# Optimization experiments

Hardware: AMD Instinct MI355X
Metric: run time of the kernel (lower is better)

Reference implementation:

```python
import jax, jax.numpy as jnp
import numpy as np

EPS = 1e-08


def _l2norm(x):
    return x / (jnp.linalg.norm(x, axis=-1, keepdims=True) + EPS)


def _mlp(x, weights):
    # weights: list of (W, b); gelu between layers, none after last
    n = len(weights)
    for i, (W, b) in enumerate(weights):
        x = x @ W + b
        if i < n - 1:
            x = jax.nn.gelu(x)  # approximate gelu, matches jax.nn.gelu default
    return x


def setup_inputs() -> dict:
    key = jax.random.key(0)
    ks = jax.random.split(key, 16)
    N, A, L, K = 65536, 32, 256, 1024
    enc_dims = [A, 512, 1024, L]
    dec_dims = [L, 1024, 512, A]

    def lin(k, din, dout):
        kw, kb = jax.random.split(k)
        W = jax.random.normal(kw, (din, dout), jnp.float32) / np.sqrt(din)
        b = jnp.zeros((dout,), jnp.float32)
        return W, b

    inp = {}
    inp["action"] = jax.random.normal(ks[0], (N, A), jnp.float32)
    inp["dim_weights"] = jax.random.uniform(ks[1], (A,), jnp.float32)
    for i in range(3):
        W, b = lin(ks[2 + i], enc_dims[i], enc_dims[i + 1])
        inp[f"enc_w{i}"], inp[f"enc_b{i}"] = W, b
    for i in range(3):
        W, b = lin(ks[5 + i], dec_dims[i], dec_dims[i + 1])
        inp[f"dec_w{i}"], inp[f"dec_b{i}"] = W, b
    cb = jax.random.normal(ks[8], (K, L), jnp.float32) * 0.1
    inp["codebook"] = _l2norm(cb)
    return inp


def reference(action, dim_weights,
              enc_w0, enc_b0, enc_w1, enc_b1, enc_w2, enc_b2,
              dec_w0, dec_b0, dec_w1, dec_b1, dec_w2, dec_b2,
              codebook):
    enc = [(enc_w0, enc_b0), (enc_w1, enc_b1), (enc_w2, enc_b2)]
    dec = [(dec_w0, dec_b0), (dec_w1, dec_b1), (dec_w2, dec_b2)]

    z_e = _l2norm(_mlp(action, enc))                       # [N, L]
    cb = _l2norm(codebook)                                 # [K, L]
    # squared euclidean distances [N, K]
    dists = (jnp.sum(z_e * z_e, axis=-1, keepdims=True)
             - 2.0 * z_e @ cb.T
             + jnp.sum(cb * cb, axis=-1))
    code_idx = jnp.argmin(dists, axis=-1)                  # [N]
    z_q = cb[code_idx]                                     # [N, L]

    z_q_ste = z_e + jax.lax.stop_gradient(z_q - z_e)
    action_hat = _mlp(z_q_ste, dec)                        # [N, A]

    sq_err = (action - action_hat) ** 2 * dim_weights
    recon_loss = jnp.mean(sq_err)
    codebook_loss = jnp.mean((jax.lax.stop_gradient(z_e) - z_q) ** 2)
    commit_loss = jnp.mean((z_e - jax.lax.stop_gradient(z_q)) ** 2)
    return action_hat, code_idx, recon_loss, codebook_loss, commit_loss
```

## Files before the change

kernel.cpp:

```cpp
#include <hip/hip_runtime.h>
#include <math.h>

#define N_ROWS 65536

typedef short short8 __attribute__((ext_vector_type(8)));
typedef float f32x4 __attribute__((ext_vector_type(4)));

__device__ __forceinline__ float gelu_f(float x) {
  float x3 = x * x * x;
  float t = tanhf(0.7978845608028654f * (x + 0.044715f * x3));
  return 0.5f * x * (1.0f + t);
}

__device__ __forceinline__ unsigned short f2bf(float f) {
  unsigned u = __float_as_uint(f);
  unsigned r = u + 0x7fffu + ((u >> 16) & 1u);
  return (unsigned short)(r >> 16);
}
__device__ __forceinline__ float bf2f(unsigned short h) {
  return __uint_as_float(((unsigned)h) << 16);
}

__device__ __forceinline__ void split3(float v, unsigned short& p0,
                                       unsigned short& p1, unsigned short& p2) {
  p0 = f2bf(v);
  float r = v - bf2f(p0);
  p1 = f2bf(r);
  r -= bf2f(p1);
  p2 = f2bf(r);
}

__device__ __forceinline__ void split3f(float v, unsigned short& p0,
                                        unsigned short& p1, unsigned short& p2) {
  unsigned u = __float_as_uint(v);
  unsigned h0 = (u + 0x8000u) & 0xffff0000u;
  float r = v - __uint_as_float(h0);
  unsigned u1 = __float_as_uint(r);
  unsigned h1 = (u1 + 0x8000u) & 0xffff0000u;
  float r2 = r - __uint_as_float(h1);
  p0 = (unsigned short)(h0 >> 16);
  p1 = (unsigned short)(h1 >> 16);
  p2 = f2bf(r2);
}

__device__ __forceinline__ void split2f(float v, unsigned short& p0,
                                        unsigned short& p1) {
  unsigned u = __float_as_uint(v);
  unsigned h0 = (u + 0x8000u) & 0xffff0000u;
  float r = v - __uint_as_float(h0);
  p0 = (unsigned short)(h0 >> 16);
  p1 = f2bf(r);
}

__device__ __forceinline__ f32x4 mfma16(short8 a, short8 b, f32x4 c) {
  return __builtin_amdgcn_mfma_f32_16x16x32_bf16(a, b, c, 0, 0, 0);
}

template <bool GELU>
__global__ __launch_bounds__(256) void gemm_kernel(
    const float* __restrict__ A, const float* __restrict__ W,
    const float* __restrict__ bias, float* __restrict__ C,
    int din, int dout) {
  __shared__ float As[16][132];
  __shared__ float Ws[16][132];
  int t = threadIdx.x;
  int tx = t & 15, ty = t >> 4;
  int c0 = blockIdx.x * 128;
  int r0 = blockIdx.y * 128;

  float acc[8][8];
#pragma unroll
  for (int i = 0; i < 8; ++i)
#pragma unroll
    for (int j = 0; j < 8; ++j) acc[i][j] = 0.0f;

  int kchunks = din >> 4;
  for (int kc = 0; kc < kchunks; ++kc) {
    int k0 = kc << 4;
    __syncthreads();
#pragma unroll
    for (int it = 0; it < 2; ++it) {
      int id = t + it * 256;
      int r = id >> 2;
      int kq = (id & 3) * 4;
      float4 v = *(const float4*)&A[(long)(r0 + r) * din + (k0 + kq)];
      As[kq + 0][r] = v.x; As[kq + 1][r] = v.y;
      As[kq + 2][r] = v.z; As[kq + 3][r] = v.w;
      int k = id >> 5;
      int cq = (id & 31) * 4;
      float4 w = *(const float4*)&W[(long)(k0 + k) * dout + (c0 + cq)];
      *(float4*)&Ws[k][cq] = w;
    }
    __syncthreads();
#pragma unroll
    for (int k = 0; k < 16; ++k) {
      float av[8], bv[8];
      *(float4*)&av[0] = *(const float4*)&As[k][ty * 4];
      *(float4*)&av[4] = *(const float4*)&As[k][ty * 4 + 64];
      *(float4*)&bv[0] = *(const float4*)&Ws[k][tx * 4];
      *(float4*)&bv[4] = *(const float4*)&Ws[k][tx * 4 + 64];
#pragma unroll
      for (int i = 0; i < 8; ++i)
#pragma unroll
        for (int j = 0; j < 8; ++j)
          acc[i][j] = fmaf(av[i], bv[j], acc[i][j]);
    }
  }

  float bbv[8];
  *(float4*)&bbv[0] = *(const float4*)&bias[c0 + tx * 4];
  *(float4*)&bbv[4] = *(const float4*)&bias[c0 + tx * 4 + 64];
#pragma unroll
  for (int i = 0; i < 8; ++i) {
    long row = r0 + ty * 4 + (i & 3) + ((i >> 2) * 64);
    float o[8];
#pragma unroll
    for (int j = 0; j < 8; ++j) {
      float v = acc[i][j] + bbv[j];
      o[j] = GELU ? gelu_f(v) : v;
    }
    *(float4*)&C[row * dout + c0 + tx * 4] = *(float4*)&o[0];
    *(float4*)&C[row * dout + c0 + tx * 4 + 64] = *(float4*)&o[4];
  }
}

template <bool GELU>
__global__ __launch_bounds__(256) void gemm64_kernel(
    const float* __restrict__ A, const float* __restrict__ W,
    const float* __restrict__ bias, float* __restrict__ C,
    int din, int dout) {
  __shared__ float As[16][68];
  __shared__ float Ws[16][68];
  int t = threadIdx.x;
  int tx = t & 15, ty = t >> 4;
  int c0 = blockIdx.x * 64;
  int r0 = blockIdx.y * 64;

  float acc[4][4];
#pragma unroll
  for (int i = 0; i < 4; ++i)
#pragma unroll
    for (int j = 0; j < 4; ++j) acc[i][j] = 0.0f;

  int kchunks = din >> 4;
  for (int kc = 0; kc < kchunks; ++kc) {
    int k0 = kc << 4;
    __syncthreads();
    {
      int r = t >> 2, kq = (t & 3) * 4;
      float4 v = *(const float4*)&A[(long)(r0 + r) * din + (k0 + kq)];
      As[kq + 0][r] = v.x; As[kq + 1][r] = v.y;
      As[kq + 2][r] = v.z; As[kq + 3][r] = v.w;
      int k = t >> 4, cq = (t & 15) * 4;
      *(float4*)&Ws[k][cq] = *(const float4*)&W[(long)(k0 + k) * dout + (c0 + cq)];
    }
    __syncthreads();
#pragma unroll
    for (int k = 0; k < 16; ++k) {
      float av[4], bv[4];
      *(float4*)&av[0] = *(const float4*)&As[k][ty * 4];
      *(float4*)&bv[0] = *(const float4*)&Ws[k][tx * 4];
#pragma unroll
      for (int i = 0; i < 4; ++i)
#pragma unroll
        for (int j = 0; j < 4; ++j)
          acc[i][j] = fmaf(av[i], bv[j], acc[i][j]);
    }
  }

  float4 bb = *(const float4*)&bias[c0 + tx * 4];
#pragma unroll
  for (int i = 0; i < 4; ++i) {
    long row = r0 + ty * 4 + i;
    float o[4];
    o[0] = acc[i][0] + bb.x; o[1] = acc[i][1] + bb.y;
    o[2] = acc[i][2] + bb.z; o[3] = acc[i][3] + bb.w;
    if (GELU) {
      o[0] = gelu_f(o[0]); o[1] = gelu_f(o[1]);
      o[2] = gelu_f(o[2]); o[3] = gelu_f(o[3]);
    }
    *(float4*)&C[row * dout + c0 + tx * 4] = *(float4*)&o[0];
  }
}

__global__ void frag_pack_kernel(const float* __restrict__ W,
                                 unsigned short* __restrict__ Bf,
                                 int K, int N) {
  int l = threadIdx.x;
  int m = l & 15, q = l >> 4;
  int cb = blockIdx.x, kb = blockIdx.y;
  unsigned short s0[8], s1[8], s2[8];
#pragma unroll
  for (int j = 0; j < 8; ++j) {
    float v = W[(long)(kb * 32 + q * 8 + j) * N + cb * 16 + m];
    split3(v, s0[j], s1[j], s2[j]);
  }
  size_t base = ((size_t)cb * (K / 32) + kb) * 3 * 512;
  *(short8*)&Bf[base + 0 * 512 + l * 8] = *(short8*)s0;
  *(short8*)&Bf[base + 1 * 512 + l * 8] = *(short8*)s1;
  *(short8*)&Bf[base + 2 * 512 + l * 8] = *(short8*)s2;
}

__global__ void frag_pack2_t(const float* __restrict__ cbn,
                             unsigned short* __restrict__ Bf) {
  int l = threadIdx.x;
  int m = l & 15, q = l >> 4;
  int cb = blockIdx.x, kb = blockIdx.y;
  unsigned short s0[8], s1[8];
  const float* src = cbn + (long)(cb * 16 + m) * 256 + kb * 32 + q * 8;
#pragma unroll
  for (int j = 0; j < 8; ++j) split2f(src[j], s0[j], s1[j]);
  size_t base = ((size_t)(cb * 8 + kb) * 2) * 512;
  *(short8*)&Bf[base + l * 8] = *(short8*)s0;
  *(short8*)&Bf[base + 512 + l * 8] = *(short8*)s1;
}

template <bool GELU>
__global__ __launch_bounds__(256) void mfma3_gemm(
    const float* __restrict__ A, const unsigned short* __restrict__ Bf,
    const float* __restrict__ bias, float* __restrict__ C,
    int K, int dout) {
  __shared__ unsigned short A_f[3 * 2 * 4 * 512];
  int t = threadIdx.x;
  int lane = t & 63, wave = t >> 6;
  int q = lane >> 4, m = lane & 15;
  int wrb = wave >> 1;
  int wr = wrb * 64, wc = (wave & 1) * 64;

  int gx = gridDim.x, tot = gx * gridDim.y;
  int lin = blockIdx.y * gx + blockIdx.x;
  if (!(tot & 7)) lin = (lin & 7) * (tot >> 3) + (lin >> 3);
  int bx = lin % gx, by = lin / gx;

  long r0 = (long)by * 128;
  int c0 = bx * 128;
  int kchunks = K >> 5;

  f32x4 acc[4][4];
#pragma unroll
  for (int i = 0; i < 4; ++i)
#pragma unroll
    for (int j = 0; j < 4; ++j) acc[i][j] = (f32x4){0.f, 0.f, 0.f, 0.f};

  int rs = t >> 1, hs = (t & 1) * 16;
  const float* aptr = A + (r0 + rs) * K + hs;
  int cb0 = (c0 + wc) >> 4;
  int xw = (rs >> 4) & 3, wrbw = rs >> 6, mw = rs & 15;
  int g0 = ((t & 1) * 2 + 0) * 16 + mw;
  int g1 = ((t & 1) * 2 + 1) * 16 + mw;
  int wb0 = (0 * 2 + wrbw) * 4 + xw;
  int wb1 = (1 * 2 + wrbw) * 4 + xw;
  int wb2 = (2 * 2 + wrbw) * 4 + xw;

  for (int kb = 0; kb < kchunks; ++kb) {
    __syncthreads();
    {
      int kt = kb << 5;
      float fv[16];
      *(float4*)&fv[0] = *(const float4*)(aptr + kt + 0);
      *(float4*)&fv[4] = *(const float4*)(aptr + kt + 4);
      *(float4*)&fv[8] = *(const float4*)(aptr + kt + 8);
      *(float4*)&fv[12] = *(const float4*)(aptr + kt + 12);
      unsigned short a0[16], a1[16], a2[16];
#pragma unroll
      for (int i = 0; i < 16; ++i) split3f(fv[i], a0[i], a1[i], a2[i]);
      *(uint4*)&A_f[wb0 * 512 + g0 * 8] = ((uint4*)a0)[0];
      *(uint4*)&A_f[wb0 * 512 + g1 * 8] = ((uint4*)a0)[1];
      *(uint4*)&A_f[wb1 * 512 + g0 * 8] = ((uint4*)a1)[0];
      *(uint4*)&A_f[wb1 * 512 + g1 * 8] = ((uint4*)a1)[1];
      *(uint4*)&A_f[wb2 * 512 + g0 * 8] = ((uint4*)a2)[0];
      *(uint4*)&A_f[wb2 * 512 + g1 * 8] = ((uint4*)a2)[1];
    }
    __syncthreads();
    short8 af[3][4];
#pragma unroll
    for (int p = 0; p < 3; ++p)
#pragma unroll
      for (int x = 0; x < 4; ++x)
        af[p][x] = *(const short8*)&A_f[((p * 2 + wrb) * 4 + x) * 512 + lane * 8];
#pragma unroll
    for (int ct = 0; ct < 4; ++ct) {
      size_t fb = ((size_t)(cb0 + ct) * kchunks + kb) * 3 * 512 + lane * 8;
      short8 b0 = *(const short8*)&Bf[fb];
      short8 b1 = *(const short8*)&Bf[fb + 512];
      short8 b2 = *(const short8*)&Bf[fb + 1024];
#pragma unroll
      for (int rt = 0; rt < 4; ++rt) {
        acc[rt][ct] = mfma16(af[0][rt], b0, acc[rt][ct]);
        acc[rt][ct] = mfma16(af[0][rt], b1, acc[rt][ct]);
        acc[rt][ct] = mfma16(af[1][rt], b0, acc[rt][ct]);
        acc[rt][ct] = mfma16(af[0][rt], b2, acc[rt][ct]);
        acc[rt][ct] = mfma16(af[1][rt], b1, acc[rt][ct]);
        acc[rt][ct] = mfma16(af[2][rt], b0, acc[rt][ct]);
      }
    }
  }

#pragma unroll
  for (int ct = 0; ct < 4; ++ct) {
    long col = c0 + wc + ct * 16 + m;
    float bv = bias[col];
#pragma unroll
    for (int rt = 0; rt < 4; ++rt) {
      long rowb = r0 + wr + rt * 16 + q * 4;
#pragma unroll
      for (int r = 0; r < 4; ++r) {
        float v = acc[rt][ct][r] + bv;
        if (GELU) v = gelu_f(v);
        C[(rowb + r) * dout + col] = v;
      }
    }
  }
}

__global__ __launch_bounds__(512) void mfma3_norm(
    const float* __restrict__ A, const unsigned short* __restrict__ Bf,
    const float* __restrict__ bias, float* __restrict__ z_e,
    float* __restrict__ ze2) {
  __shared__ unsigned short A_f[3 * 2 * 4 * 512];
  __shared__ float S[128][4];
  __shared__ float Sinv[128];
  const int K = 1024, kchunks = 32;
  int t = threadIdx.x;
  int lane = t & 63, wave = t >> 6;
  int q = lane >> 4, m = lane & 15;
  int wrb = wave >> 2;
  int wcq = wave & 3;
  long r0 = (long)blockIdx.x * 128;

  f32x4 acc[4][4];
#pragma unroll
  for (int i = 0; i < 4; ++i)
#pragma unroll
    for (int j = 0; j < 4; ++j) acc[i][j] = (f32x4){0.f, 0.f, 0.f, 0.f};

  int rs = t >> 2, kq = t & 3;
  const float* aptr = A + (r0 + rs) * K + kq * 8;
  int xw = (rs >> 4) & 3, wrbw = rs >> 6, mw = rs & 15;
  int gw = kq * 16 + mw;
  int wb0 = (0 * 2 + wrbw) * 4 + xw;
  int wb1 = (1 * 2 + wrbw) * 4 + xw;
  int wb2 = (2 * 2 + wrbw) * 4 + xw;
  int cb0 = wcq * 4;

  for (int kb = 0; kb < kchunks; ++kb) {
    __syncthreads();
    {
      float fv[8];
      *(float4*)&fv[0] = *(const float4*)(aptr + (kb << 5));
      *(float4*)&fv[4] = *(const float4*)(aptr + (kb << 5) + 4);
      unsigned short a0[8], a1[8], a2[8];
#pragma unroll
      for (int i = 0; i < 8; ++i) split3f(fv[i], a0[i], a1[i], a2[i]);
      *(uint4*)&A_f[wb0 * 512 + gw * 8] = *(uint4*)a0;
      *(uint4*)&A_f[wb1 * 512 + gw * 8] = *(uint4*)a1;
      *(uint4*)&A_f[wb2 * 512 + gw * 8] = *(uint4*)a2;
    }
    __syncthreads();
    short8 af[3][4];
#pragma unroll
    for (int p = 0; p < 3; ++p)
#pragma unroll
      for (int x = 0; x < 4; ++x)
        af[p][x] = *(const short8*)&A_f[((p * 2 + wrb) * 4 + x) * 512 + lane * 8];
#pragma unroll
    for (int ct = 0; ct < 4; ++ct) {
      size_t fb = ((size_t)(cb0 + ct) * kchunks + kb) * 3 * 512 + lane * 8;
      short8 b0 = *(const short8*)&Bf[fb];
      short8 b1 = *(const short8*)&Bf[fb + 512];
      short8 b2 = *(const short8*)&Bf[fb + 1024];
#pragma unroll
      for (int rt = 0; rt < 4; ++rt) {
        acc[rt][ct] = mfma16(af[0][rt], b0, acc[rt][ct]);
        acc[rt][ct] = mfma16(af[0][rt], b1, acc[rt][ct]);
        acc[rt][ct] = mfma16(af[1][rt], b0, acc[rt][ct]);
        acc[rt][ct] = mfma16(af[0][rt], b2, acc[rt][ct]);
        acc[rt][ct] = mfma16(af[1][rt], b1, acc[rt][ct]);
        acc[rt][ct] = mfma16(af[2][rt], b0, acc[rt][ct]);
      }
    }
  }

#pragma unroll
  for (int ct = 0; ct < 4; ++ct) {
    float bv = bias[wcq * 64 + ct * 16 + m];
#pragma unroll
    for (int rt = 0; rt < 4; ++rt)
#pragma unroll
      for (int r = 0; r < 4; ++r) acc[rt][ct][r] += bv;
  }

#pragma unroll
  for (int rt = 0; rt < 4; ++rt)
#pragma unroll
    for (int r = 0; r < 4; ++r) {
      float s = acc[rt][0][r] * acc[rt][0][r] + acc[rt][1][r] * acc[rt][1][r] +
                acc[rt][2][r] * acc[rt][2][r] + acc[rt][3][r] * acc[rt][3][r];
#pragma unroll
      for (int off = 1; off <= 8; off <<= 1) s += __shfl_xor(s, off);
      if (m == 0) S[wrb * 64 + rt * 16 + q * 4 + r][wcq] = s;
    }
  __syncthreads();
  if (t < 128) {
    float s = S[t][0] + S[t][1] + S[t][2] + S[t][3];
    float den = sqrtf(s) + 1e-8f;
    Sinv[t] = 1.0f / den;
    ze2[r0 + t] = s / (den * den);
  }
  __syncthreads();
#pragma unroll
  for (int rt = 0; rt < 4; ++rt)
#pragma unroll
    for (int r = 0; r < 4; ++r) {
      int rl = wrb * 64 + rt * 16 + q * 4 + r;
      float inv = Sinv[rl];
#pragma unroll
      for (int ct = 0; ct < 4; ++ct)
        z_e[(r0 + rl) * 256 + wcq * 64 + ct * 16 + m] = acc[rt][ct][r] * inv;
    }
}

__global__ __launch_bounds__(256) void dist2_mfma(
    const float* __restrict__ z_e, const unsigned short* __restrict__ cbf,
    int* __restrict__ idxc, int* __restrict__ fixcnt, int* __restrict__ fixlist) {
  __shared__ unsigned short A_f[2 * 8 * 4 * 512];
  __shared__ float Lv1[64][4], Lv2[64][4];
  __shared__ int Lc1[64][4];
  int t = threadIdx.x;
  int lane = t & 63, wave = t >> 6;
  int q = lane >> 4, m = lane & 15;
  long r0 = (long)blockIdx.x * 64;

#pragma unroll
  for (int it = 0; it < 4; ++it) {
    int kb = it * 2 + (t >> 7);
    int rs = (t & 127) >> 1, hs = (t & 1) * 16;
    const float* ap = z_e + (r0 + rs) * 256 + kb * 32 + hs;
    float fv[16];
    *(float4*)&fv[0] = *(const float4*)(ap + 0);
    *(float4*)&fv[4] = *(const float4*)(ap + 4);
    *(float4*)&fv[8] = *(const float4*)(ap + 8);
    *(float4*)&fv[12] = *(const float4*)(ap + 12);
    unsigned short a0[16], a1[16];
#pragma unroll
    for (int i = 0; i < 16; ++i) split2f(fv[i], a0[i], a1[i]);
    int x = rs >> 4, mm = rs & 15;
    int ga = ((t & 1) * 2 + 0) * 16 + mm;
    int gb = ((t & 1) * 2 + 1) * 16 + mm;
    int b0 = ((0 * 8 + kb) * 4 + x) * 512;
    int b1 = ((1 * 8 + kb) * 4 + x) * 512;
    *(uint4*)&A_f[b0 + ga * 8] = ((uint4*)a0)[0];
    *(uint4*)&A_f[b0 + gb * 8] = ((uint4*)a0)[1];
    *(uint4*)&A_f[b1 + ga * 8] = ((uint4*)a1)[0];
    *(uint4*)&A_f[b1 + gb * 8] = ((uint4*)a1)[1];
  }
  __syncthreads();

  float v1[4][4], v2[4][4];
  int c1[4][4];
#pragma unroll
  for (int i = 0; i < 4; ++i)
#pragma unroll
    for (int j = 0; j < 4; ++j) { v1[i][j] = -3.4e38f; v2[i][j] = -3.4e38f; c1[i][j] = 0; }

  for (int ctp = 0; ctp < 4; ++ctp) {
    f32x4 acc[4][4];
#pragma unroll
    for (int i = 0; i < 4; ++i)
#pragma unroll
      for (int j = 0; j < 4; ++j) acc[i][j] = (f32x4){0.f, 0.f, 0.f, 0.f};

    for (int kb = 0; kb < 8; ++kb) {
      short8 af0[4], af1[4];
#pragma unroll
      for (int rt = 0; rt < 4; ++rt) {
        af0[rt] = *(const short8*)&A_f[((0 * 8 + kb) * 4 + rt) * 512 + lane * 8];
        af1[rt] = *(const short8*)&A_f[((1 * 8 + kb) * 4 + rt) * 512 + lane * 8];
      }
      short8 bf0[4], bf1[4];
#pragma unroll
      for (int cs = 0; cs < 4; ++cs) {
        int cb = ctp * 16 + (cs >> 1) * 8 + wave * 2 + (cs & 1);
        size_t fb = ((size_t)(cb * 8 + kb) * 2) * 512 + lane * 8;
        bf0[cs] = *(const short8*)&cbf[fb];
        bf1[cs] = *(const short8*)&cbf[fb + 512];
      }
#pragma unroll
      for (int rt = 0; rt < 4; ++rt)
#pragma unroll
        for (int cs = 0; cs < 4; ++cs) {
          acc[rt][cs] = mfma16(af0[rt], bf0[cs], acc[rt][cs]);
          acc[rt][cs] = mfma16(af0[rt], bf1[cs], acc[rt][cs]);
          acc[rt][cs] = mfma16(af1[rt], bf0[cs], acc[rt][cs]);
        }
    }
#pragma unroll
    for (int rt = 0; rt < 4; ++rt)
#pragma unroll
      for (int cs = 0; cs < 4; ++cs) {
        int colb = ctp * 256 + (cs >> 1) * 128 + wave * 32 + (cs & 1) * 16 + m;
#pragma unroll
        for (int r = 0; r < 4; ++r) {
          float v = acc[rt][cs][r];
          float nv2 = fmaxf(v2[rt][r], fminf(v, v1[rt][r]));
          if (v > v1[rt][r]) { c1[rt][r] = colb; v1[rt][r] = v; }
          v2[rt][r] = nv2;
        }
      }
  }

#pragma unroll
  for (int off = 1; off <= 8; off <<= 1) {
#pragma unroll
    for (int rt = 0; rt < 4; ++rt)
#pragma unroll
      for (int r = 0; r < 4; ++r) {
        float ov1 = __shfl_xor(v1[rt][r], off);
        float ov2 = __shfl_xor(v2[rt][r], off);
        int oc1 = __shfl_xor(c1[rt][r], off);
        float nv2 = fmaxf(fmaxf(v2[rt][r], ov2), fminf(v1[rt][r], ov1));
        if (ov1 > v1[rt][r] || (ov1 == v1[rt][r] && oc1 < c1[rt][r])) {
          v1[rt][r] = ov1; c1[rt][r] = oc1;
        }
        v2[rt][r] = nv2;
      }
  }
  if (m == 0) {
#pragma unroll
    for (int rt = 0; rt < 4; ++rt)
#pragma unroll
      for (int r = 0; r < 4; ++r) {
        int rloc = rt * 16 + q * 4 + r;
        Lv1[rloc][wave] = v1[rt][r];
        Lv2[rloc][wave] = v2[rt][r];
        Lc1[rloc][wave] = c1[rt][r];
      }
  }
  __syncthreads();
  if (t < 64) {
    float a1 = Lv1[t][0], a2 = Lv2[t][0];
    int ac = Lc1[t][0];
#pragma unroll
    for (int w = 1; w < 4; ++w) {
      float b1 = Lv1[t][w], b2 = Lv2[t][w];
      int bc = Lc1[t][w];
      float n2 = fmaxf(fmaxf(a2, b2), fminf(a1, b1));
      if (b1 > a1 || (b1 == a1 && bc < ac)) { a1 = b1; ac = bc; }
      a2 = n2;
    }
    idxc[r0 + t] = ac;
    if (a1 - a2 < 5.0e-4f) {
      int p = atomicAdd(fixcnt, 1);
      fixlist[p] = r0 + t;
    }
  }
}

__global__ __launch_bounds__(256) void fixup_part(
    const float* __restrict__ z_e, const float* __restrict__ cbn,
    const float* __restrict__ ze2, const float* __restrict__ cb2,
    const int* __restrict__ fixlist, const int* __restrict__ fixcnt,
    float* __restrict__ fixbv, int* __restrict__ fixbc) {
  int cnt = *fixcnt;
  int r0 = blockIdx.y * 128;
  if (r0 >= cnt) return;
  int ctile = blockIdx.x;
  int c0 = ctile * 128;
  __shared__ float As[16][132];
  __shared__ float Ws[16][132];
  __shared__ float rv[128][17];
  __shared__ int rc[128][17];
  __shared__ int rows_l[128];
  int t = threadIdx.x, tx = t & 15, ty = t >> 4;

  if (t < 128) rows_l[t] = fixlist[(r0 + t < cnt) ? (r0 + t) : 0];
  __syncthreads();

  float bestv[8];
  int bestc[8];
  float myze2[8];
#pragma unroll
  for (int i = 0; i < 8; ++i) {
    bestv[i] = 3.4e38f;
    bestc[i] = 0;
    int rl = ty * 4 + (i & 3) + ((i >> 2) * 64);
    myze2[i] = ze2[rows_l[rl]];
  }

  float acc[8][8];
#pragma unroll
  for (int i = 0; i < 8; ++i)
#pragma unroll
    for (int j = 0; j < 8; ++j) acc[i][j] = 0.0f;

  for (int kc = 0; kc < 16; ++kc) {
    int k0 = kc << 4;
    __syncthreads();
#pragma unroll
    for (int it = 0; it < 2; ++it) {
      int id = t + it * 256;
      int r = id >> 2;
      int kq = (id & 3) * 4;
      float4 v = *(const float4*)&z_e[(long)rows_l[r] * 256 + k0 + kq];
      As[kq + 0][r] = v.x; As[kq + 1][r] = v.y;
      As[kq + 2][r] = v.z; As[kq + 3][r] = v.w;
      float4 w = *(const float4*)&cbn[(long)(c0 + r) * 256 + k0 + kq];
      Ws[kq + 0][r] = w.x; Ws[kq + 1][r] = w.y;
      Ws[kq + 2][r] = w.z; Ws[kq + 3][r] = w.w;
    }
    __syncthreads();
#pragma unroll
    for (int k = 0; k < 16; ++k) {
      float av[8], bv[8];
      *(float4*)&av[0] = *(const float4*)&As[k][ty * 4];
      *(float4*)&av[4] = *(const float4*)&As[k][ty * 4 + 64];
      *(float4*)&bv[0] = *(const float4*)&Ws[k][tx * 4];
      *(float4*)&bv[4] = *(const float4*)&Ws[k][tx * 4 + 64];
#pragma unroll
      for (int i = 0; i < 8; ++i)
#pragma unroll
        for (int j = 0; j < 8; ++j)
          acc[i][j] = fmaf(av[i], bv[j], acc[i][j]);
    }
  }

  float cb2v[8];
  *(float4*)&cb2v[0] = *(const float4*)&cb2[c0 + tx * 4];
  *(float4*)&cb2v[4] = *(const float4*)&cb2[c0 + tx * 4 + 64];
#pragma unroll
  for (int i = 0; i < 8; ++i)
#pragma unroll
    for (int j = 0; j < 8; ++j) {
      int c = c0 + tx * 4 + (j & 3) + ((j >> 2) * 64);
      float d = (myze2[i] - 2.0f * acc[i][j]) + cb2v[j];
      if (d < bestv[i] || (d == bestv[i] && c < bestc[i])) {
        bestv[i] = d;
        bestc[i] = c;
      }
    }

  __syncthreads();
#pragma unroll
  for (int i = 0; i < 8; ++i) {
    int rl = ty * 4 + (i & 3) + ((i >> 2) * 64);
    rv[rl][tx] = bestv[i];
    rc[rl][tx] = bestc[i];
  }
  __syncthreads();
  if (t < 128 && r0 + t < cnt) {
    float bv = rv[t][0];
    int bc = rc[t][0];
    for (int j = 1; j < 16; ++j) {
      float v = rv[t][j];
      int c = rc[t][j];
      if (v < bv || (v == bv && c < bc)) { bv = v; bc = c; }
    }
    fixbv[(long)(r0 + t) * 8 + ctile] = bv;
    fixbc[(long)(r0 + t) * 8 + ctile] = bc;
  }
}

__global__ __launch_bounds__(256) void fixup_reduce(
    const float* __restrict__ fixbv, const int* __restrict__ fixbc,
    const int* __restrict__ fixlist, const int* __restrict__ fixcnt,
    int* __restrict__ idxc) {
  int cnt = *fixcnt;
  int i = blockIdx.x * 256 + threadIdx.x;
  if (i >= cnt) return;
  float bv = fixbv[(long)i * 8];
  int bc = fixbc[(long)i * 8];
#pragma unroll
  for (int j = 1; j < 8; ++j) {
    float v = fixbv[(long)i * 8 + j];
    int c = fixbc[(long)i * 8 + j];
    if (v < bv || (v == bv && c < bc)) { bv = v; bc = c; }
  }
  idxc[fixlist[i]] = bc;
}

__global__ __launch_bounds__(256) void rownorm_kernel(
    const float* __restrict__ in, float* __restrict__ outv,
    float* __restrict__ outsq) {
  int wid = threadIdx.x >> 6, lane = threadIdx.x & 63;
  long row = (long)blockIdx.x * 4 + wid;
  const float* src = in + row * 256;
  float4 v = *(const float4*)&src[lane * 4];
  float s = v.x * v.x + v.y * v.y + v.z * v.z + v.w * v.w;
#pragma unroll
  for (int off = 32; off >= 1; off >>= 1) s += __shfl_xor(s, off);
  float denom = sqrtf(s) + 1e-8f;
  float4 o;
  o.x = v.x / denom; o.y = v.y / denom; o.z = v.z / denom; o.w = v.w / denom;
  *(float4*)&outv[row * 256 + lane * 4] = o;
  float s2 = o.x * o.x + o.y * o.y + o.z * o.z + o.w * o.w;
#pragma unroll
  for (int off = 32; off >= 1; off >>= 1) s2 += __shfl_xor(s2, off);
  if (lane == 0) outsq[row] = s2;
}

__global__ __launch_bounds__(256) void t2_kernel(
    const float* __restrict__ T1, const float* __restrict__ W,
    const float* __restrict__ bias, float* __restrict__ T2) {
  int id = blockIdx.x * 256 + threadIdx.x;
  int row = id >> 5, col = id & 31;
  const float* a = T1 + (long)row * 512;
  float s = 0.f;
#pragma unroll 8
  for (int k = 0; k < 512; ++k) s = fmaf(a[k], W[k * 32 + col], s);
  T2[id] = s + bias[col];
}

__global__ __launch_bounds__(256) void fused_tail(
    const float* __restrict__ z_e, const float* __restrict__ cbn,
    const int* __restrict__ idxc, const float* __restrict__ T2,
    const float* __restrict__ action, const float* __restrict__ dimw,
    float* __restrict__ partRe, float* __restrict__ partCo,
    float* __restrict__ outIdx, float* __restrict__ ahat, int pb) {
  int t = threadIdx.x, wid = t >> 6, lane = t & 63;
  float cs = 0.f, rsum = 0.f;
#pragma unroll
  for (int r = 0; r < 4; ++r) {
    long row = (long)blockIdx.x * 16 + wid * 4 + r;
    int k = idxc[row];
    float4 a = *(const float4*)&z_e[row * 256 + lane * 4];
    float4 b = *(const float4*)&cbn[(long)k * 256 + lane * 4];
    float dx = a.x - b.x, dy = a.y - b.y, dz = a.z - b.z, dq = a.w - b.w;
    cs += dx * dx + dy * dy + dz * dz + dq * dq;
    if (lane < 8) {
      float4 av = *(const float4*)&action[row * 32 + lane * 4];
      float4 tv = *(const float4*)&T2[(long)k * 32 + lane * 4];
      float4 wv = *(const float4*)&dimw[lane * 4];
      *(float4*)&ahat[row * 32 + lane * 4] = tv;
      float ex = av.x - tv.x, ey = av.y - tv.y;
      float ez = av.z - tv.z, ew = av.w - tv.w;
      rsum += ex * ex * wv.x + ey * ey * wv.y + ez * ez * wv.z + ew * ew * wv.w;
    }
    if (lane == 0) outIdx[row] = (float)k;
  }
#pragma unroll
  for (int off = 32; off >= 1; off >>= 1) {
    cs += __shfl_xor(cs, off);
    rsum += __shfl_xor(rsum, off);
  }
  __shared__ float rc[4], rr[4];
  if (lane == 0) { rc[wid] = cs; rr[wid] = rsum; }
  __syncthreads();
  if (t == 0) {
    partCo[pb + blockIdx.x] = rc[0] + rc[1] + rc[2] + rc[3];
    partRe[pb + blockIdx.x] = rr[0] + rr[1] + rr[2] + rr[3];
  }
}

__global__ void zero_kernel(int* __restrict__ cnts) {
  if (threadIdx.x < 32) cnts[threadIdx.x] = 0;
}

__global__ __launch_bounds__(256) void finalize_kernel(
    const float* __restrict__ partRe, const float* __restrict__ partCo,
    float* __restrict__ out) {
  int t = threadIdx.x;
  float sr = 0.f, sc = 0.f;
  for (int i = t; i < 4096; i += 256) { sr += partRe[i]; sc += partCo[i]; }
#pragma unroll
  for (int off = 32; off >= 1; off >>= 1) {
    sr += __shfl_xor(sr, off);
    sc += __shfl_xor(sc, off);
  }
  __shared__ float rs_[4], cs_[4];
  int wid = t >> 6, lane = t & 63;
  if (lane == 0) { rs_[wid] = sr; cs_[wid] = sc; }
  __syncthreads();
  if (t == 0) {
    float r = rs_[0] + rs_[1] + rs_[2] + rs_[3];
    float c = cs_[0] + cs_[1] + cs_[2] + cs_[3];
    out[0] = r / (65536.0f * 32.0f);
    float cl = c / (65536.0f * 256.0f);
    out[1] = cl;
    out[2] = cl;
  }
}

extern "C" void kernel_launch(void* const* d_in, const int* in_sizes, int n_in,
                              void* d_out, int out_size, void* d_ws,
                              size_t ws_size, hipStream_t stream) {
  const float* action = (const float*)d_in[0];
  const float* dimw = (const float*)d_in[1];
  const float* ew0 = (const float*)d_in[2];
  const float* eb0 = (const float*)d_in[3];
  const float* ew1 = (const float*)d_in[4];
  const float* eb1 = (const float*)d_in[5];
  const float* ew2 = (const float*)d_in[6];
  const float* eb2 = (const float*)d_in[7];
  const float* dw0 = (const float*)d_in[8];
  const float* db0 = (const float*)d_in[9];
  const float* dw1 = (const float*)d_in[10];
  const float* db1 = (const float*)d_in[11];
  const float* dw2 = (const float*)d_in[12];
  const float* db2 = (const float*)d_in[13];
  const float* cb = (const float*)d_in[14];
  float* out = (float*)d_out;
  char* ws = (char*)d_ws;

  const size_t fixed_b = 1048576 + 4096 + 1048576 + 3145728 + 1572864 +
                         4194304 + 2097152 + 131072 + 256 + 32768;
  int R = N_ROWS;
  while (R > 2048) {
    if (fixed_b + (size_t)R * 6220 + 65536 <= ws_size) break;
    R >>= 1;
  }

  size_t off = 0;
  float* cbn = (float*)(ws + off); off += 1048576;
  float* cb2 = (float*)(ws + off); off += 4096;
  unsigned short* cbf = (unsigned short*)(ws + off); off += 1048576;
  unsigned short* ewf1 = (unsigned short*)(ws + off); off += 3145728;
  unsigned short* ewf2 = (unsigned short*)(ws + off); off += 1572864;
  float* T0 = (float*)(ws + off); off += 4194304;
  float* T1d = (float*)(ws + off); off += 2097152;
  float* T2d = (float*)(ws + off); off += 131072;
  int* fixcnts = (int*)(ws + off); off += 256;
  float* partRe = (float*)(ws + off); off += 16384;
  float* partCo = (float*)(ws + off); off += 16384;
  float* ze2 = (float*)(ws + off); off += (size_t)R * 4;
  int* idxc = (int*)(ws + off); off += (size_t)R * 4;
  int* fixlist = (int*)(ws + off); off += (size_t)R * 4;
  float* fixbv = (float*)(ws + off); off += (size_t)R * 32;
  int* fixbc = (int*)(ws + off); off += (size_t)R * 32;
  char* P0 = ws + off; off += (size_t)R * 2048;
  char* P1 = ws + off; off += (size_t)R * 4096;

  float* e0 = (float*)P0;
  float* e1 = (float*)P1;
  float* z_e = (float*)(P0 + (size_t)R * 1024);

  zero_kernel<<<1, 64, 0, stream>>>(fixcnts);
  rownorm_kernel<<<256, 256, 0, stream>>>(cb, cbn, cb2);
  frag_pack2_t<<<dim3(64, 8), 64, 0, stream>>>(cbn, cbf);
  frag_pack_kernel<<<dim3(64, 16), 64, 0, stream>>>(ew1, ewf1, 512, 1024);
  frag_pack_kernel<<<dim3(16, 32), 64, 0, stream>>>(ew2, ewf2, 1024, 256);

  gemm64_kernel<true><<<dim3(16, 16), 256, 0, stream>>>(cbn, dw0, db0, T0, 256, 1024);
  gemm64_kernel<true><<<dim3(8, 16), 256, 0, stream>>>(T0, dw1, db1, T1d, 1024, 512);
  t2_kernel<<<128, 256, 0, stream>>>(T1d, dw2, db2, T2d);

  for (int base = 0; base < N_ROWS; base += R) {
    int ci = base / R;
    const float* act_c = action + (size_t)base * 32;
    float* out_c = out + (size_t)base * 32;
    int* fixcnt = &fixcnts[ci];

    gemm_kernel<true><<<dim3(4, R / 128), 256, 0, stream>>>(
        act_c, ew0, eb0, e0, 32, 512);
    mfma3_gemm<true><<<dim3(8, R / 128), 256, 0, stream>>>(
        e0, ewf1, eb1, e1, 512, 1024);
    mfma3_norm<<<R / 128, 512, 0, stream>>>(e1, ewf2, eb2, z_e, ze2);

    dist2_mfma<<<R / 64, 256, 0, stream>>>(z_e, cbf, idxc, fixcnt, fixlist);
    fixup_part<<<dim3(8, R / 128), 256, 0, stream>>>(
        z_e, cbn, ze2, cb2, fixlist, fixcnt, fixbv, fixbc);
    fixup_reduce<<<R / 256, 256, 0, stream>>>(fixbv, fixbc, fixlist, fixcnt,
                                              idxc);

    fused_tail<<<R / 16, 256, 0, stream>>>(
        z_e, cbn, idxc, T2d, act_c, dimw, partRe, partCo,
        out + 2097152 + base, out_c, base >> 4);
  }

  finalize_kernel<<<1, 256, 0, stream>>>(partRe, partCo, out + 2162688);
}
```

Before: 1.179 ms.

## Emit pre-split bf16 planes from first encoder layer and shrink norm block tile

The first encoder GEMM now applies GELU and splits its output into three bf16 planes in global memory. The second-layer MFMA GEMM loads those planes directly instead of reading fp32 and splitting each K-chunk again in every column block, which removes work that was repeated across the 8 column blocks. Separately, the normalizing layer-3 kernel now uses 64-row, 256-thread blocks instead of 128-row, 512-thread blocks, giving more blocks and less LDS per block. The trade is larger intermediate storage (3x16-bit instead of 32-bit per element), so the workspace sizing and z_e aliasing are adjusted.

```diff
diff --git a/kernel.cpp b/kernel.cpp
--- a/kernel.cpp
+++ b/kernel.cpp
@@ -56,11 +56,10 @@
   return __builtin_amdgcn_mfma_f32_16x16x32_bf16(a, b, c, 0, 0, 0);
 }
 
-template <bool GELU>
-__global__ __launch_bounds__(256) void gemm_kernel(
+__global__ __launch_bounds__(256) void gemm_enc0_split(
     const float* __restrict__ A, const float* __restrict__ W,
-    const float* __restrict__ bias, float* __restrict__ C,
-    int din, int dout) {
+    const float* __restrict__ bias, unsigned short* __restrict__ P,
+    size_t aps, int din, int dout) {
   __shared__ float As[16][132];
   __shared__ float Ws[16][132];
   int t = threadIdx.x;
@@ -113,14 +112,26 @@
 #pragma unroll
   for (int i = 0; i < 8; ++i) {
     long row = r0 + ty * 4 + (i & 3) + ((i >> 2) * 64);
-    float o[8];
+    unsigned short s0[8], s1[8], s2[8];
 #pragma unroll
     for (int j = 0; j < 8; ++j) {
-      float v = acc[i][j] + bbv[j];
-      o[j] = GELU ? gelu_f(v) : v;
-    }
-    *(float4*)&C[row * dout + c0 + tx * 4] = *(float4*)&o[0];
-    *(float4*)&C[row * dout + c0 + tx * 4 + 64] = *(float4*)&o[4];
+      float v = gelu_f(acc[i][j] + bbv[j]);
+      split3f(v, s0[j], s1[j], s2[j]);
+    }
+    size_t b = (size_t)row * dout + c0 + tx * 4;
+    ushort4 w;
+    w.x = s0[0]; w.y = s0[1]; w.z = s0[2]; w.w = s0[3];
+    *(ushort4*)&P[b] = w;
+    w.x = s0[4]; w.y = s0[5]; w.z = s0[6]; w.w = s0[7];
+    *(ushort4*)&P[b + 64] = w;
+    w.x = s1[0]; w.y = s1[1]; w.z = s1[2]; w.w = s1[3];
+    *(ushort4*)&P[aps + b] = w;
+    w.x = s1[4]; w.y = s1[5]; w.z = s1[6]; w.w = s1[7];
+    *(ushort4*)&P[aps + b + 64] = w;
+    w.x = s2[0]; w.y = s2[1]; w.z = s2[2]; w.w = s2[3];
+    *(ushort4*)&P[2 * aps + b] = w;
+    w.x = s2[4]; w.y = s2[5]; w.z = s2[6]; w.w = s2[7];
+    *(ushort4*)&P[2 * aps + b + 64] = w;
   }
 }
 
@@ -217,7 +228,8 @@
 
 template <bool GELU>
 __global__ __launch_bounds__(256) void mfma3_gemm(
-    const float* __restrict__ A, const unsigned short* __restrict__ Bf,
+    const unsigned short* __restrict__ Ap, size_t aps,
+    const unsigned short* __restrict__ Bf,
     const float* __restrict__ bias, float* __restrict__ C,
     int K, int dout) {
   __shared__ unsigned short A_f[3 * 2 * 4 * 512];
@@ -243,7 +255,9 @@
     for (int j = 0; j < 4; ++j) acc[i][j] = (f32x4){0.f, 0.f, 0.f, 0.f};
 
   int rs = t >> 1, hs = (t & 1) * 16;
-  const float* aptr = A + (r0 + rs) * K + hs;
+  const unsigned short* a0p = Ap + (size_t)(r0 + rs) * K + hs;
+  const unsigned short* a1p = a0p + aps;
+  const unsigned short* a2p = a0p + 2 * aps;
   int cb0 = (c0 + wc) >> 4;
   int xw = (rs >> 4) & 3, wrbw = rs >> 6, mw = rs & 15;
   int g0 = ((t & 1) * 2 + 0) * 16 + mw;
@@ -256,20 +270,18 @@
     __syncthreads();
     {
       int kt = kb << 5;
-      float fv[16];
-      *(float4*)&fv[0] = *(const float4*)(aptr + kt + 0);
-      *(float4*)&fv[4] = *(const float4*)(aptr + kt + 4);
-      *(float4*)&fv[8] = *(const float4*)(aptr + kt + 8);
-      *(float4*)&fv[12] = *(const float4*)(aptr + kt + 12);
-      unsigned short a0[16], a1[16], a2[16];
-#pragma unroll
-      for (int i = 0; i < 16; ++i) split3f(fv[i], a0[i], a1[i], a2[i]);
-      *(uint4*)&A_f[wb0 * 512 + g0 * 8] = ((uint4*)a0)[0];
-      *(uint4*)&A_f[wb0 * 512 + g1 * 8] = ((uint4*)a0)[1];
-      *(uint4*)&A_f[wb1 * 512 + g0 * 8] = ((uint4*)a1)[0];
-      *(uint4*)&A_f[wb1 * 512 + g1 * 8] = ((uint4*)a1)[1];
-      *(uint4*)&A_f[wb2 * 512 + g0 * 8] = ((uint4*)a2)[0];
-      *(uint4*)&A_f[wb2 * 512 + g1 * 8] = ((uint4*)a2)[1];
+      uint4 u00 = *(const uint4*)(a0p + kt);
+      uint4 u01 = *(const uint4*)(a0p + kt + 8);
+      uint4 u10 = *(const uint4*)(a1p + kt);
+      uint4 u11 = *(const uint4*)(a1p + kt + 8);
+      uint4 u20 = *(const uint4*)(a2p + kt);
+      uint4 u21 = *(const uint4*)(a2p + kt + 8);
+      *(uint4*)&A_f[wb0 * 512 + g0 * 8] = u00;
+      *(uint4*)&A_f[wb0 * 512 + g1 * 8] = u01;
+      *(uint4*)&A_f[wb1 * 512 + g0 * 8] = u10;
+      *(uint4*)&A_f[wb1 * 512 + g1 * 8] = u11;
+      *(uint4*)&A_f[wb2 * 512 + g0 * 8] = u20;
+      *(uint4*)&A_f[wb2 * 512 + g1 * 8] = u21;
     }
     __syncthreads();
     short8 af[3][4];
@@ -313,20 +325,18 @@
   }
 }
 
-__global__ __launch_bounds__(512) void mfma3_norm(
+__global__ __launch_bounds__(256) void mfma3_norm(
     const float* __restrict__ A, const unsigned short* __restrict__ Bf,
     const float* __restrict__ bias, float* __restrict__ z_e,
     float* __restrict__ ze2) {
-  __shared__ unsigned short A_f[3 * 2 * 4 * 512];
-  __shared__ float S[128][4];
-  __shared__ float Sinv[128];
+  __shared__ unsigned short A_f[3 * 4 * 512];
+  __shared__ float S[64][4];
+  __shared__ float Sinv[64];
   const int K = 1024, kchunks = 32;
   int t = threadIdx.x;
   int lane = t & 63, wave = t >> 6;
   int q = lane >> 4, m = lane & 15;
-  int wrb = wave >> 2;
-  int wcq = wave & 3;
-  long r0 = (long)blockIdx.x * 128;
+  long r0 = (long)blockIdx.x * 64;
 
   f32x4 acc[4][4];
 #pragma unroll
@@ -336,12 +346,10 @@
 
   int rs = t >> 2, kq = t & 3;
   const float* aptr = A + (r0 + rs) * K + kq * 8;
-  int xw = (rs >> 4) & 3, wrbw = rs >> 6, mw = rs & 15;
+  int xw = rs >> 4, mw = rs & 15;
   int gw = kq * 16 + mw;
-  int wb0 = (0 * 2 + wrbw) * 4 + xw;
-  int wb1 = (1 * 2 + wrbw) * 4 + xw;
-  int wb2 = (2 * 2 + wrbw) * 4 + xw;
-  int cb0 = wcq * 4;
+  int wb0 = 0 * 4 + xw, wb1 = 1 * 4 + xw, wb2 = 2 * 4 + xw;
+  int cb0 = wave * 4;
 
   for (int kb = 0; kb < kchunks; ++kb) {
     __syncthreads();
@@ -362,7 +370,7 @@
     for (int p = 0; p < 3; ++p)
 #pragma unroll
       for (int x = 0; x < 4; ++x)
-        af[p][x] = *(const short8*)&A_f[((p * 2 + wrb) * 4 + x) * 512 + lane * 8];
+        af[p][x] = *(const short8*)&A_f[(p * 4 + x) * 512 + lane * 8];
 #pragma unroll
     for (int ct = 0; ct < 4; ++ct) {
       size_t fb = ((size_t)(cb0 + ct) * kchunks + kb) * 3 * 512 + lane * 8;
@@ -383,7 +391,7 @@
 
 #pragma unroll
   for (int ct = 0; ct < 4; ++ct) {
-    float bv = bias[wcq * 64 + ct * 16 + m];
+    float bv = bias[wave * 64 + ct * 16 + m];
 #pragma unroll
     for (int rt = 0; rt < 4; ++rt)
 #pragma unroll
@@ -398,10 +406,10 @@
                 acc[rt][2][r] * acc[rt][2][r] + acc[rt][3][r] * acc[rt][3][r];
 #pragma unroll
       for (int off = 1; off <= 8; off <<= 1) s += __shfl_xor(s, off);
-      if (m == 0) S[wrb * 64 + rt * 16 + q * 4 + r][wcq] = s;
+      if (m == 0) S[rt * 16 + q * 4 + r][wave] = s;
     }
   __syncthreads();
-  if (t < 128) {
+  if (t < 64) {
     float s = S[t][0] + S[t][1] + S[t][2] + S[t][3];
     float den = sqrtf(s) + 1e-8f;
     Sinv[t] = 1.0f / den;
@@ -412,11 +420,11 @@
   for (int rt = 0; rt < 4; ++rt)
 #pragma unroll
     for (int r = 0; r < 4; ++r) {
-      int rl = wrb * 64 + rt * 16 + q * 4 + r;
+      int rl = rt * 16 + q * 4 + r;
       float inv = Sinv[rl];
 #pragma unroll
       for (int ct = 0; ct < 4; ++ct)
-        z_e[(r0 + rl) * 256 + wcq * 64 + ct * 16 + m] = acc[rt][ct][r] * inv;
+        z_e[(r0 + rl) * 256 + wave * 64 + ct * 16 + m] = acc[rt][ct][r] * inv;
     }
 }
 
@@ -805,7 +813,7 @@
                          4194304 + 2097152 + 131072 + 256 + 32768;
   int R = N_ROWS;
   while (R > 2048) {
-    if (fixed_b + (size_t)R * 6220 + 65536 <= ws_size) break;
+    if (fixed_b + (size_t)R * 7244 + 65536 <= ws_size) break;
     R >>= 1;
   }
 
@@ -826,12 +834,13 @@
   int* fixlist = (int*)(ws + off); off += (size_t)R * 4;
   float* fixbv = (float*)(ws + off); off += (size_t)R * 32;
   int* fixbc = (int*)(ws + off); off += (size_t)R * 32;
-  char* P0 = ws + off; off += (size_t)R * 2048;
+  char* P0 = ws + off; off += (size_t)R * 3072;
   char* P1 = ws + off; off += (size_t)R * 4096;
 
-  float* e0 = (float*)P0;
+  unsigned short* e0p = (unsigned short*)P0;
+  size_t aps0 = (size_t)R * 512;
   float* e1 = (float*)P1;
-  float* z_e = (float*)(P0 + (size_t)R * 1024);
+  float* z_e = (float*)P0;
 
   zero_kernel<<<1, 64, 0, stream>>>(fixcnts);
   rownorm_kernel<<<256, 256, 0, stream>>>(cb, cbn, cb2);
@@ -849,11 +858,11 @@
     float* out_c = out + (size_t)base * 32;
     int* fixcnt = &fixcnts[ci];
 
-    gemm_kernel<true><<<dim3(4, R / 128), 256, 0, stream>>>(
-        act_c, ew0, eb0, e0, 32, 512);
+    gemm_enc0_split<<<dim3(4, R / 128), 256, 0, stream>>>(
+        act_c, ew0, eb0, e0p, aps0, 32, 512);
     mfma3_gemm<true><<<dim3(8, R / 128), 256, 0, stream>>>(
-        e0, ewf1, eb1, e1, 512, 1024);
-    mfma3_norm<<<R / 128, 512, 0, stream>>>(e1, ewf2, eb2, z_e, ze2);
+        e0p, aps0, ewf1, eb1, e1, 512, 1024);
+    mfma3_norm<<<R / 64, 256, 0, stream>>>(e1, ewf2, eb2, z_e, ze2);
 
     dist2_mfma<<<R / 64, 256, 0, stream>>>(z_e, cbf, idxc, fixcnt, fixlist);
     fixup_part<<<dim3(8, R / 128), 256, 0, stream>>>(
```

New measurement: 1.155 ms. 1.02x faster.
